# Performance work log

Measured on AMD Instinct MI355X. Metric: run time of the kernel, lower is better.

Reference implementation:

```python
import jax, jax.numpy as jnp
import numpy as np

L = 512      # number of grid points
B = 32768    # batch of independent trajectories


def _rhs(y, w):
    # y: [4, B] -> dy: [4, B]; tiny coupled polynomial vector field
    A, T, N, C = y
    dA = w[0] + w[1] * A + w[2] * A ** 2
    dT = w[3] + w[4] * T + w[5] * T ** 2 + w[6] * A + w[7] * A ** 2 + w[8] * A * T
    dN = w[9] + w[10] * N + w[11] * N ** 2 + w[12] * T + w[13] * T ** 2 + w[14] * T * N
    dC = w[15] + w[16] * C + w[17] * C ** 2 + w[18] * N + w[19] * N ** 2 + w[20] * N * C
    return jnp.stack([dA, dT, dN, dC])


def setup_inputs() -> dict:
    key = jax.random.key(0)
    k1, k2 = jax.random.split(key)
    s_grid = jnp.arange(L, dtype=jnp.float32) * 0.01  # increasing grid, small h
    y0 = jax.random.normal(k1, (4, B), dtype=jnp.float32)
    w = jax.random.normal(k2, (21,), dtype=jnp.float32) * 0.001  # nn.Parameter init
    return {"s_grid": s_grid, "y0": y0, "w": w}


def reference(s_grid, y0, w):
    hs = jnp.diff(s_grid)  # [L-1] step sizes h_i = s[i] - s[i-1]

    def step(y, h):
        y_next = y + h * _rhs(y, w)  # explicit Euler
        return y_next, y_next

    _, ys = jax.lax.scan(step, y0, hs)          # [L-1, 4, B]
    return jnp.concatenate([y0[None], ys], 0)   # [L, 4, B]
```

## Files before the change

kernel.cpp:

```cpp
#include <hip/hip_runtime.h>
#include <hip/hip_bf16.h>


#define ODE_L 512
#define ODE_B 32768

__global__ __launch_bounds__(64) void population_ode_kernel(
    const float* __restrict__ s_grid,
    const float* __restrict__ y0,
    const float* __restrict__ w,
    float* __restrict__ out)
{
    __shared__ float sh_s[ODE_L];

    const int tid = threadIdx.x;
    #pragma unroll
    for (int i = tid; i < ODE_L; i += 64) {
        sh_s[i] = s_grid[i];
    }

    const float w0  = w[0],  w1  = w[1],  w2  = w[2];
    const float w3  = w[3],  w4  = w[4],  w5  = w[5],  w6  = w[6],  w7  = w[7],  w8  = w[8];
    const float w9  = w[9],  w10 = w[10], w11 = w[11], w12 = w[12], w13 = w[13], w14 = w[14];
    const float w15 = w[15], w16 = w[16], w17 = w[17], w18 = w[18], w19 = w[19], w20 = w[20];

    __syncthreads();

    const int b = blockIdx.x * 64 + tid;

    float A = y0[0 * ODE_B + b];
    float T = y0[1 * ODE_B + b];
    float N = y0[2 * ODE_B + b];
    float C = y0[3 * ODE_B + b];

    out[0 * ODE_B + b] = A;
    out[1 * ODE_B + b] = T;
    out[2 * ODE_B + b] = N;
    out[3 * ODE_B + b] = C;

    float s_prev = sh_s[0];

    for (int i = 1; i < ODE_L; ++i) {
        const float s_cur = sh_s[i];
        const float h = s_cur - s_prev;
        s_prev = s_cur;

        const float dA = w0  + w1  * A + w2  * A * A;
        const float dT = w3  + w4  * T + w5  * T * T + w6  * A + w7  * A * A + w8  * A * T;
        const float dN = w9  + w10 * N + w11 * N * N + w12 * T + w13 * T * T + w14 * T * N;
        const float dC = w15 + w16 * C + w17 * C * C + w18 * N + w19 * N * N + w20 * N * C;

        A = A + h * dA;
        T = T + h * dT;
        N = N + h * dN;
        C = C + h * dC;

        const size_t base = (size_t)i * (4 * ODE_B) + (size_t)b;
        out[base + 0 * ODE_B] = A;
        out[base + 1 * ODE_B] = T;
        out[base + 2 * ODE_B] = N;
        out[base + 3 * ODE_B] = C;
    }
}

extern "C" void kernel_launch(void* const* d_in, const int* in_sizes, int n_in,
                              void* d_out, int out_size, void* d_ws, size_t ws_size,
                              hipStream_t stream) {
    (void)in_sizes; (void)n_in; (void)d_ws; (void)ws_size; (void)out_size;

    const float* s_grid = (const float*)d_in[0];
    const float* y0     = (const float*)d_in[1];
    const float* w      = (const float*)d_in[2];
    float* out          = (float*)d_out;

    dim3 grid(ODE_B / 64);
    dim3 block(64);
    population_ode_kernel<<<grid, block, 0, stream>>>(s_grid, y0, w, out);
}
```

Before: 273.2 us.

## Split Euler scan into checkpoint pass plus parallel segment recomputation

A first kernel integrates each trajectory serially but writes state only every 32 steps, producing checkpoints. A second kernel launches one block row per segment and recomputes the 31 intermediate steps from each checkpoint in parallel, writing the full output. The aim is to decouple the large output write traffic from the serial dependency chain so stores run with far more parallelism, at the cost of doing the arithmetic twice and adding a second launch. Recomputation repeats the exact same float operations in the same order, so results should match bitwise.

```diff
diff --git a/kernel.cpp b/kernel.cpp
--- a/kernel.cpp
+++ b/kernel.cpp
@@ -1,29 +1,46 @@
 #include <hip/hip_runtime.h>
-#include <hip/hip_bf16.h>
 
 
 #define ODE_L 512
 #define ODE_B 32768
+#define SEG   32
+#define NSEG  (ODE_L / SEG)
 
-__global__ __launch_bounds__(64) void population_ode_kernel(
+#define ODE_STEP(A, T, N, C, h)                                              \
+  do {                                                                       \
+    const float dA = w0  + w1  * A + w2  * A * A;                            \
+    const float dT = w3  + w4  * T + w5  * T * T + w6  * A + w7  * A * A +   \
+                     w8  * A * T;                                            \
+    const float dN = w9  + w10 * N + w11 * N * N + w12 * T + w13 * T * T +   \
+                     w14 * T * N;                                            \
+    const float dC = w15 + w16 * C + w17 * C * C + w18 * N + w19 * N * N +   \
+                     w20 * N * C;                                            \
+    A += h * dA; T += h * dT; N += h * dN; C += h * dC;                      \
+  } while (0)
+
+#define ODE_LOAD_W                                                            \
+  const float w0  = w[0],  w1  = w[1],  w2  = w[2];                           \
+  const float w3  = w[3],  w4  = w[4],  w5  = w[5],  w6  = w[6],  w7 = w[7], \
+              w8  = w[8];                                                     \
+  const float w9  = w[9],  w10 = w[10], w11 = w[11], w12 = w[12],             \
+              w13 = w[13], w14 = w[14];                                       \
+  const float w15 = w[15], w16 = w[16], w17 = w[17], w18 = w[18],             \
+              w19 = w[19], w20 = w[20]
+
+__global__ __launch_bounds__(64) void ode_checkpoint_kernel(
     const float* __restrict__ s_grid,
     const float* __restrict__ y0,
     const float* __restrict__ w,
     float* __restrict__ out)
 {
-    __shared__ float sh_s[ODE_L];
+    __shared__ float sh_s[ODE_L - SEG + 1];
 
     const int tid = threadIdx.x;
-    #pragma unroll
-    for (int i = tid; i < ODE_L; i += 64) {
+    for (int i = tid; i <= ODE_L - SEG; i += 64) {
         sh_s[i] = s_grid[i];
     }
 
-    const float w0  = w[0],  w1  = w[1],  w2  = w[2];
-    const float w3  = w[3],  w4  = w[4],  w5  = w[5],  w6  = w[6],  w7  = w[7],  w8  = w[8];
-    const float w9  = w[9],  w10 = w[10], w11 = w[11], w12 = w[12], w13 = w[13], w14 = w[14];
-    const float w15 = w[15], w16 = w[16], w17 = w[17], w18 = w[18], w19 = w[19], w20 = w[20];
-
+    ODE_LOAD_W;
     __syncthreads();
 
     const int b = blockIdx.x * 64 + tid;
@@ -40,22 +57,60 @@
 
     float s_prev = sh_s[0];
 
-    for (int i = 1; i < ODE_L; ++i) {
-        const float s_cur = sh_s[i];
+    for (int cp = 0; cp < NSEG - 1; ++cp) {
+        #pragma unroll
+        for (int j = 0; j < SEG; ++j) {
+            const int i = cp * SEG + j + 1;
+            const float s_cur = sh_s[i];
+            const float h = s_cur - s_prev;
+            s_prev = s_cur;
+            ODE_STEP(A, T, N, C, h);
+        }
+        const size_t base = (size_t)((cp + 1) * SEG) * (4 * ODE_B) + (size_t)b;
+        out[base + 0 * ODE_B] = A;
+        out[base + 1 * ODE_B] = T;
+        out[base + 2 * ODE_B] = N;
+        out[base + 3 * ODE_B] = C;
+    }
+}
+
+__global__ __launch_bounds__(256) void ode_segment_kernel(
+    const float* __restrict__ s_grid,
+    const float* __restrict__ w,
+    float* __restrict__ out)
+{
+    __shared__ float sh_s[SEG];
+
+    const int tid = threadIdx.x;
+    const int seg = blockIdx.y;
+    const int i0  = seg * SEG;
+
+    if (tid < SEG) {
+        sh_s[tid] = s_grid[i0 + tid];
+    }
+
+    ODE_LOAD_W;
+    __syncthreads();
+
+    const int b = blockIdx.x * 256 + tid;
+
+    const size_t base0 = (size_t)i0 * (4 * ODE_B) + (size_t)b;
+    float A = out[base0 + 0 * ODE_B];
+    float T = out[base0 + 1 * ODE_B];
+    float N = out[base0 + 2 * ODE_B];
+    float C = out[base0 + 3 * ODE_B];
+
+    float s_prev = sh_s[0];
+
+    #pragma unroll 4
+    for (int j = 1; j < SEG; ++j) {
+        const float s_cur = sh_s[j];
         const float h = s_cur - s_prev;
         s_prev = s_cur;
 
-        const float dA = w0  + w1  * A + w2  * A * A;
-        const float dT = w3  + w4  * T + w5  * T * T + w6  * A + w7  * A * A + w8  * A * T;
-        const float dN = w9  + w10 * N + w11 * N * N + w12 * T + w13 * T * T + w14 * T * N;
-        const float dC = w15 + w16 * C + w17 * C * C + w18 * N + w19 * N * N + w20 * N * C;
+        ODE_STEP(A, T, N, C, h);
 
-        A = A + h * dA;
-        T = T + h * dT;
-        N = N + h * dN;
-        C = C + h * dC;
-
-        const size_t base = (size_t)i * (4 * ODE_B) + (size_t)b;
+        const size_t base = (size_t)(i0 + j) * (4 * ODE_B) + (size_t)b;
         out[base + 0 * ODE_B] = A;
         out[base + 1 * ODE_B] = T;
         out[base + 2 * ODE_B] = N;
@@ -73,7 +128,9 @@
     const float* w      = (const float*)d_in[2];
     float* out          = (float*)d_out;
 
-    dim3 grid(ODE_B / 64);
-    dim3 block(64);
-    population_ode_kernel<<<grid, block, 0, stream>>>(s_grid, y0, w, out);
+    ode_checkpoint_kernel<<<dim3(ODE_B / 64), dim3(64), 0, stream>>>(
+        s_grid, y0, w, out);
+
+    ode_segment_kernel<<<dim3(ODE_B / 256, NSEG), dim3(256), 0, stream>>>(
+        s_grid, w, out);
 }
```

After: 288.7 us. +5.7%, slower.

## Split time axis into segments with redundant recompute and float4-packed trajectories

Applied to the files above, without the earlier changes.

Each block now owns one 32-step time segment for 1024 trajectories. It recomputes the Euler recurrence from y0 up to the segment start without storing anything, then writes only its own segment. This exposes 16x more blocks so the store-bound output write can spread across all CUs. Each thread handles 4 trajectories with float4 loads and stores, and segment order is mirrored between the two grid halves to balance the redundant compute. The cost is extra recomputation that grows with segment index, and a different floating-point evaluation order per block, though it stays the same sequence of operations.

```diff
diff --git a/kernel.cpp b/kernel.cpp
--- a/kernel.cpp
+++ b/kernel.cpp
@@ -1,65 +1,101 @@
 #include <hip/hip_runtime.h>
-#include <hip/hip_bf16.h>
 
 
 #define ODE_L 512
 #define ODE_B 32768
+#define SEG   32
+#define NSEG  (ODE_L / SEG)
+#define TPB   256
+#define PACK  4
+#define BPB   (TPB * PACK)
+#define NCOL  (ODE_B / BPB)
 
-__global__ __launch_bounds__(64) void population_ode_kernel(
+#define ODE_STEP1(A, T, N, C, h)                                             \
+  do {                                                                       \
+    const float dA = w0  + w1  * A + w2  * A * A;                            \
+    const float dT = w3  + w4  * T + w5  * T * T + w6  * A + w7  * A * A +   \
+                     w8  * A * T;                                            \
+    const float dN = w9  + w10 * N + w11 * N * N + w12 * T + w13 * T * T +   \
+                     w14 * T * N;                                            \
+    const float dC = w15 + w16 * C + w17 * C * C + w18 * N + w19 * N * N +   \
+                     w20 * N * C;                                            \
+    A += h * dA; T += h * dT; N += h * dN; C += h * dC;                      \
+  } while (0)
+
+#define ODE_STEP4(h)                                                         \
+  do {                                                                       \
+    ODE_STEP1(A0, T0, N0, C0, h);                                            \
+    ODE_STEP1(A1, T1, N1, C1, h);                                            \
+    ODE_STEP1(A2, T2, N2, C2, h);                                            \
+    ODE_STEP1(A3, T3, N3, C3, h);                                            \
+  } while (0)
+
+__global__ __launch_bounds__(TPB, 2) void ode_fused_kernel(
     const float* __restrict__ s_grid,
     const float* __restrict__ y0,
     const float* __restrict__ w,
     float* __restrict__ out)
 {
-    __shared__ float sh_s[ODE_L];
+    __shared__ float sh_h[ODE_L - 1];
 
     const int tid = threadIdx.x;
-    #pragma unroll
-    for (int i = tid; i < ODE_L; i += 64) {
-        sh_s[i] = s_grid[i];
+    for (int i = tid; i < ODE_L - 1; i += TPB) {
+        sh_h[i] = s_grid[i + 1] - s_grid[i];
     }
 
     const float w0  = w[0],  w1  = w[1],  w2  = w[2];
-    const float w3  = w[3],  w4  = w[4],  w5  = w[5],  w6  = w[6],  w7  = w[7],  w8  = w[8];
-    const float w9  = w[9],  w10 = w[10], w11 = w[11], w12 = w[12], w13 = w[13], w14 = w[14];
-    const float w15 = w[15], w16 = w[16], w17 = w[17], w18 = w[18], w19 = w[19], w20 = w[20];
+    const float w3  = w[3],  w4  = w[4],  w5  = w[5],  w6  = w[6],  w7 = w[7],
+                w8  = w[8];
+    const float w9  = w[9],  w10 = w[10], w11 = w[11], w12 = w[12],
+                w13 = w[13], w14 = w[14];
+    const float w15 = w[15], w16 = w[16], w17 = w[17], w18 = w[18],
+                w19 = w[19], w20 = w[20];
 
     __syncthreads();
 
-    const int b = blockIdx.x * 64 + tid;
+    const int bid  = blockIdx.x;
+    const int half = bid >> 8;
+    const int idx  = bid & 255;
+    const int seg  = half ? (15 - (idx & 15)) : (idx & 15);
+    const int col  = (idx >> 4) + (half << 4);
+    const int b0   = col * BPB + tid * PACK;
 
-    float A = y0[0 * ODE_B + b];
-    float T = y0[1 * ODE_B + b];
-    float N = y0[2 * ODE_B + b];
-    float C = y0[3 * ODE_B + b];
+    float4 vA = *reinterpret_cast<const float4*>(&y0[0 * ODE_B + b0]);
+    float4 vT = *reinterpret_cast<const float4*>(&y0[1 * ODE_B + b0]);
+    float4 vN = *reinterpret_cast<const float4*>(&y0[2 * ODE_B + b0]);
+    float4 vC = *reinterpret_cast<const float4*>(&y0[3 * ODE_B + b0]);
 
-    out[0 * ODE_B + b] = A;
-    out[1 * ODE_B + b] = T;
-    out[2 * ODE_B + b] = N;
-    out[3 * ODE_B + b] = C;
+    float A0 = vA.x, A1 = vA.y, A2 = vA.z, A3 = vA.w;
+    float T0 = vT.x, T1 = vT.y, T2 = vT.z, T3 = vT.w;
+    float N0 = vN.x, N1 = vN.y, N2 = vN.z, N3 = vN.w;
+    float C0 = vC.x, C1 = vC.y, C2 = vC.z, C3 = vC.w;
 
-    float s_prev = sh_s[0];
+    for (int c = 0; c < seg; ++c) {
+        const int base_h = c * SEG;
+        #pragma unroll 8
+        for (int j = 0; j < SEG; ++j) {
+            const float h = sh_h[base_h + j];
+            ODE_STEP4(h);
+        }
+    }
 
-    for (int i = 1; i < ODE_L; ++i) {
-        const float s_cur = sh_s[i];
-        const float h = s_cur - s_prev;
-        s_prev = s_cur;
-
-        const float dA = w0  + w1  * A + w2  * A * A;
-        const float dT = w3  + w4  * T + w5  * T * T + w6  * A + w7  * A * A + w8  * A * T;
-        const float dN = w9  + w10 * N + w11 * N * N + w12 * T + w13 * T * T + w14 * T * N;
-        const float dC = w15 + w16 * C + w17 * C * C + w18 * N + w19 * N * N + w20 * N * C;
-
-        A = A + h * dA;
-        T = T + h * dT;
-        N = N + h * dN;
-        C = C + h * dC;
-
-        const size_t base = (size_t)i * (4 * ODE_B) + (size_t)b;
-        out[base + 0 * ODE_B] = A;
-        out[base + 1 * ODE_B] = T;
-        out[base + 2 * ODE_B] = N;
-        out[base + 3 * ODE_B] = C;
+    const int i0 = seg * SEG;
+    {
+        const size_t base = (size_t)i0 * (4 * ODE_B) + (size_t)b0;
+        *reinterpret_cast<float4*>(&out[base + 0 * ODE_B]) = make_float4(A0, A1, A2, A3);
+        *reinterpret_cast<float4*>(&out[base + 1 * ODE_B]) = make_float4(T0, T1, T2, T3);
+        *reinterpret_cast<float4*>(&out[base + 2 * ODE_B]) = make_float4(N0, N1, N2, N3);
+        *reinterpret_cast<float4*>(&out[base + 3 * ODE_B]) = make_float4(C0, C1, C2, C3);
+    }
+    #pragma unroll 8
+    for (int j = 1; j < SEG; ++j) {
+        const float h = sh_h[i0 + j - 1];
+        ODE_STEP4(h);
+        const size_t base = (size_t)(i0 + j) * (4 * ODE_B) + (size_t)b0;
+        *reinterpret_cast<float4*>(&out[base + 0 * ODE_B]) = make_float4(A0, A1, A2, A3);
+        *reinterpret_cast<float4*>(&out[base + 1 * ODE_B]) = make_float4(T0, T1, T2, T3);
+        *reinterpret_cast<float4*>(&out[base + 2 * ODE_B]) = make_float4(N0, N1, N2, N3);
+        *reinterpret_cast<float4*>(&out[base + 3 * ODE_B]) = make_float4(C0, C1, C2, C3);
     }
 }
 
@@ -73,7 +109,6 @@
     const float* w      = (const float*)d_in[2];
     float* out          = (float*)d_out;
 
-    dim3 grid(ODE_B / 64);
-    dim3 block(64);
-    population_ode_kernel<<<grid, block, 0, stream>>>(s_grid, y0, w, out);
+    ode_fused_kernel<<<dim3(NSEG * NCOL), dim3(TPB), 0, stream>>>(
+        s_grid, y0, w, out);
 }
```

After: 303.1 us. +10.9%, slower.
